# Kernel tuning notes

Hardware: AMD Instinct MI355X
Metric: run time of the kernel (lower is better)

The kernel has to match this reference:

```python
import jax, jax.numpy as jnp
import numpy as np

N = 100000      # nodes
E = 2500000     # edges
DIN, H, DOUT = 3, 32, 4
EPS = 1e-5

def _lin(k, i, o):
    kw, kb = jax.random.split(k)
    lim = 1.0 / np.sqrt(i)
    W = jax.random.uniform(kw, (i, o), jnp.float32, -lim, lim)
    b = jax.random.uniform(kb, (o,), jnp.float32, -lim, lim)
    return W, b

def setup_inputs():
    key = jax.random.key(0)
    ks = jax.random.split(key, 12)
    x = jax.random.normal(ks[0], (N, DIN), jnp.float32)
    edge_index = jax.random.randint(ks[1], (2, E), 0, N, dtype=jnp.int32)
    w_in1, b_in1 = _lin(ks[2], DIN, H)
    w_in2, b_in2 = _lin(ks[3], H, H)
    gamma = jnp.ones((H,), jnp.float32)
    beta = jnp.zeros((H,), jnp.float32)
    wg1, bg1 = _lin(ks[4], H, H)
    wg2, bg2 = _lin(ks[5], H, H)
    wg3, bg3 = _lin(ks[6], H, H)
    wo1, bo1 = _lin(ks[7], H, H)
    wo2, bo2 = _lin(ks[8], H, H)
    wo3, bo3 = _lin(ks[9], H, DOUT)
    return dict(x=x, w_in1=w_in1, b_in1=b_in1, w_in2=w_in2, b_in2=b_in2,
                gamma=gamma, beta=beta,
                wg1=wg1, bg1=bg1, wg2=wg2, bg2=bg2, wg3=wg3, bg3=bg3,
                wo1=wo1, bo1=bo1, wo2=wo2, bo2=bo2, wo3=wo3, bo3=bo3,
                edge_index=edge_index)

def _gcn(h, W, b, src, dst, norm):
    # PyG GCNConv: x' = scatter_add(norm * (xW)[src] -> dst) + bias
    hw = h @ W                                   # [N, H]
    msg = hw[src] * norm[:, None]                # [E+N, H] gather + scale
    out = jax.ops.segment_sum(msg, dst, num_segments=N)
    return out + b

def reference(x, w_in1, b_in1, w_in2, b_in2, gamma, beta,
              wg1, bg1, wg2, bg2, wg3, bg3,
              wo1, bo1, wo2, bo2, wo3, bo3, edge_index):
    leaky = lambda v: jax.nn.leaky_relu(v, 0.01)
    # input MLP
    h = leaky(x @ w_in1 + b_in1)
    h = leaky(h @ w_in2 + b_in2)
    # BatchNorm1d (training-mode batch statistics, biased variance)
    mu = jnp.mean(h, axis=0)
    var = jnp.mean((h - mu) ** 2, axis=0)
    h = (h - mu) * jax.lax.rsqrt(var + EPS) * gamma + beta
    # gcn_norm with self-loops: deg over target index, sym normalization
    loop = jnp.arange(N, dtype=edge_index.dtype)
    src = jnp.concatenate([edge_index[0], loop])
    dst = jnp.concatenate([edge_index[1], loop])
    deg = jax.ops.segment_sum(jnp.ones_like(src, jnp.float32), dst, num_segments=N)
    dis = jax.lax.rsqrt(deg)                     # deg >= 1 due to self-loops
    norm = dis[src] * dis[dst]                   # [E+N]
    h = jax.nn.elu(_gcn(h, wg1, bg1, src, dst, norm))
    h = jax.nn.elu(_gcn(h, wg2, bg2, src, dst, norm))
    h = jax.nn.elu(_gcn(h, wg3, bg3, src, dst, norm))
    # output MLP
    r = leaky(h @ wo1 + bo1)
    r = leaky(r @ wo2 + bo2)
    r = r @ wo3 + bo3                            # [N, 4]
    r = r.at[:, 0].set(jax.nn.sigmoid(r[:, 0]))
    return r
```

## Files before the change

kernel.cpp:

```cpp
#include <hip/hip_runtime.h>
#include <hip/hip_fp16.h>

#define HF 32
#define EPS 1e-5f
#define BSH 7
#define BSZ 128
#define CH  16384
#define SUBCAP 512
#define CAP (8*SUBCAP)

typedef int vi4 __attribute__((ext_vector_type(4)));

__device__ __forceinline__ float leaky(float v){ return fmaxf(v, 0.01f*v); }
__device__ __forceinline__ float elu1(float v){ return v > 0.f ? v : (expf(v)-1.f); }
__device__ __forceinline__ float sigmoidf(float v){ return 1.f/(1.f+expf(-v)); }

__device__ __forceinline__ int4 nt_load_i4(const int* p){
    vi4 v = __builtin_nontemporal_load((const vi4*)p);
    return make_int4(v.x, v.y, v.z, v.w);
}

__device__ __forceinline__ void addrow8(float* a, float4 v){
    const __half2* p = (const __half2*)&v;
#pragma unroll
    for (int k = 0; k < 4; k++){
        float2 f = __half22float2(p[k]);
        a[2*k] += f.x; a[2*k+1] += f.y;
    }
}
__device__ __forceinline__ float4 h2add4f(float4 a, float4 b){
    __half2* pa = (__half2*)&a; __half2* pb = (__half2*)&b;
    float4 r; __half2* pr = (__half2*)&r;
#pragma unroll
    for (int k = 0; k < 4; k++) pr[k] = __hadd2(pa[k], pb[k]);
    return r;
}

union SMem {
    struct {
        float sW1[3*HF]; float sB1[HF]; float sW2[HF*HF]; float sB2[HF];
        float sh[256][33];
    } mlp;
    struct { int lcnt[1024]; int lbase[1024]; int lpos[1024]; } bin;
};

__global__ __launch_bounds__(256)
void k_mlp_bin(const float* __restrict__ x,
               const float* __restrict__ w1, const float* __restrict__ b1,
               const float* __restrict__ w2, const float* __restrict__ b2,
               __half* __restrict__ h, float* __restrict__ stats,
               const int* __restrict__ src, const int* __restrict__ dst,
               int* __restrict__ gfill, int* __restrict__ ep,
               int N, int E, int B, int NB1){
    __shared__ SMem sm;
    int t = threadIdx.x;
    if ((int)blockIdx.x < NB1){
        for (int i = t; i < 3*HF; i += 256) sm.mlp.sW1[i] = w1[i];
        if (t < HF){ sm.mlp.sB1[t] = b1[t]; sm.mlp.sB2[t] = b2[t]; }
        for (int i = t; i < HF*HF; i += 256) sm.mlp.sW2[i] = w2[i];
        __syncthreads();
        int n = blockIdx.x*256 + t;
        float h2[HF];
        if (n < N){
            float x0 = x[(size_t)n*3], x1 = x[(size_t)n*3+1], x2 = x[(size_t)n*3+2];
            float h1[HF];
#pragma unroll
            for (int j = 0; j < HF; j++){
                float v = fmaf(x0, sm.mlp.sW1[j], fmaf(x1, sm.mlp.sW1[HF+j],
                          fmaf(x2, sm.mlp.sW1[2*HF+j], sm.mlp.sB1[j])));
                h1[j] = leaky(v);
            }
#pragma unroll
            for (int j = 0; j < HF; j++){
                float v = sm.mlp.sB2[j];
#pragma unroll
                for (int i = 0; i < HF; i++) v = fmaf(h1[i], sm.mlp.sW2[i*HF+j], v);
                h2[j] = leaky(v);
            }
            float4* hv = (float4*)(h + (size_t)n*HF);
#pragma unroll
            for (int jb = 0; jb < 4; jb++){
                __half2 hh[4];
#pragma unroll
                for (int k = 0; k < 4; k++)
                    hh[k] = __float22half2_rn(make_float2(h2[jb*8+2*k], h2[jb*8+2*k+1]));
                hv[jb] = *(float4*)hh;
            }
        } else {
#pragma unroll
            for (int j = 0; j < HF; j++) h2[j] = 0.f;
        }
#pragma unroll
        for (int j = 0; j < HF; j++) sm.mlp.sh[t][j] = h2[j];
        __syncthreads();
        int f = t & 31, g = t >> 5;
        float s = 0.f, ss = 0.f;
        for (int i = 0; i < 32; i++){
            float v = sm.mlp.sh[g*32 + i][f];
            s += v; ss += v*v;
        }
        __syncthreads();
        sm.mlp.sh[g][f] = s; sm.mlp.sh[8+g][f] = ss;
        __syncthreads();
        if (t < HF){
            float a = 0.f, b = 0.f;
#pragma unroll
            for (int g2 = 0; g2 < 8; g2++){ a += sm.mlp.sh[g2][t]; b += sm.mlp.sh[8+g2][t]; }
            atomicAdd(&stats[t], a);
            atomicAdd(&stats[HF+t], b);
        }
    } else {
        int bid = blockIdx.x - NB1;
        for (int i = t; i < B; i += 256){ sm.bin.lcnt[i] = 0; sm.bin.lpos[i] = 0; }
        __syncthreads();
        int base = bid * CH;
        int xcd = blockIdx.x & 7;
        bool full = (base + CH <= E);
        if (full){
            for (int i = 0; i < 16; i++){
                int4 d4 = nt_load_i4(dst + base + (t + i*256)*4);
                atomicAdd(&sm.bin.lcnt[d4.x >> BSH], 1);
                atomicAdd(&sm.bin.lcnt[d4.y >> BSH], 1);
                atomicAdd(&sm.bin.lcnt[d4.z >> BSH], 1);
                atomicAdd(&sm.bin.lcnt[d4.w >> BSH], 1);
            }
        } else {
            for (int i = 0; i < 64; i++){
                int e = base + t + i*256;
                if (e < E) atomicAdd(&sm.bin.lcnt[dst[e] >> BSH], 1);
            }
        }
        __syncthreads();
        for (int i = t; i < B; i += 256){
            int c = sm.bin.lcnt[i];
            sm.bin.lbase[i] = c ? (i*CAP + xcd*SUBCAP + atomicAdd(&gfill[i*8 + xcd], c)) : 0;
        }
        __syncthreads();
        if (full){
            for (int i = 0; i < 16; i++){
                int idx = base + (t + i*256)*4;
                int4 d4 = *(const int4*)(dst + idx);
                int4 s4 = *(const int4*)(src + idx);
                int dd[4] = {d4.x, d4.y, d4.z, d4.w};
                int ss[4] = {s4.x, s4.y, s4.z, s4.w};
#pragma unroll
                for (int k = 0; k < 4; k++){
                    int bb = dd[k] >> BSH;
                    int p = sm.bin.lbase[bb] + atomicAdd(&sm.bin.lpos[bb], 1);
                    ep[p] = (ss[k] << BSH) | (dd[k] & (BSZ-1));
                }
            }
        } else {
            for (int i = 0; i < 64; i++){
                int e = base + t + i*256;
                if (e < E){
                    int d = dst[e], s = src[e];
                    int bb = d >> BSH;
                    int p = sm.bin.lbase[bb] + atomicAdd(&sm.bin.lpos[bb], 1);
                    ep[p] = (s << BSH) | (d & (BSZ-1));
                }
            }
        }
    }
}

__global__ __launch_bounds__(256)
void k_csr_t1(int* __restrict__ ep, const int* __restrict__ gfill,
              int2* __restrict__ rowp2, float* __restrict__ dis,
              const __half* __restrict__ h, const float* __restrict__ stats,
              const float* __restrict__ gamma, const float* __restrict__ beta,
              const float* __restrict__ W, __half* __restrict__ tout,
              int N, int B){
    __shared__ int sep[CAP];
    __shared__ int lcnt[128], lpre[128], lfill[128];
    __shared__ float sW[HF*HF];
    __shared__ float sscale[HF], sshift[HF];
    int t = threadIdx.x;
    int b = blockIdx.x;
    for (int i = t; i < HF*HF; i += 256) sW[i] = W[i];
    if (t < HF){
        float inv = 1.0f/(float)N;
        float mu  = stats[t]*inv;
        float var = stats[HF+t]*inv - mu*mu;
        float rs  = rsqrtf(var + EPS);
        float sc  = rs*gamma[t];
        sscale[t] = sc;
        sshift[t] = beta[t] - mu*sc;
    }
    if (t < 128){ lcnt[t] = 0; lfill[t] = 0; }
    int cx[8], coff[8], cnt = 0;
#pragma unroll
    for (int xx = 0; xx < 8; xx++){ cx[xx] = gfill[b*8 + xx]; coff[xx] = cnt; cnt += cx[xx]; }
    int base = b*CAP;
    __syncthreads();
#pragma unroll
    for (int xx = 0; xx < 8; xx++)
        for (int j = t; j < cx[xx]; j += 256) sep[coff[xx] + j] = ep[base + xx*SUBCAP + j];
    __syncthreads();
    for (int e = t; e < cnt; e += 256) atomicAdd(&lcnt[sep[e] & (BSZ-1)], 1);
    __syncthreads();
    if (t < 128){
        int dg = lcnt[t];
        int pre = 0;
        for (int j = 0; j < t; j++) pre += lcnt[j];
        lpre[t] = pre;
        int n = b*BSZ + t;
        if (n < N){
            rowp2[n] = make_int2(base + pre, base + pre + dg);
            dis[n]   = rsqrtf((float)dg + 1.0f);
        }
    }
    __syncthreads();
    for (int e = t; e < cnt; e += 256){
        int val = sep[e];
        int d = val & (BSZ-1);
        int p = lpre[d] + atomicAdd(&lfill[d], 1);
        ep[base + p] = val >> BSH;
    }
    int nloc = t >> 1, fh = (t & 1) * 16;
    int n = b*BSZ + nloc;
    if (n < N){
        float dloc = rsqrtf((float)lcnt[nloc] + 1.0f);
        const float4* hv4 = (const float4*)h + (size_t)n*4;
        float v[HF];
#pragma unroll
        for (int k = 0; k < 4; k++){
            float4 raw = hv4[k];
            const __half2* p2 = (const __half2*)&raw;
#pragma unroll
            for (int q = 0; q < 4; q++){
                float2 f2 = __half22float2(p2[q]);
                v[8*k + 2*q]     = f2.x;
                v[8*k + 2*q + 1] = f2.y;
            }
        }
#pragma unroll
        for (int f = 0; f < HF; f++) v[f] = fmaf(v[f], sscale[f], sshift[f]);
        float o[16];
#pragma unroll
        for (int j = 0; j < 16; j++) o[j] = 0.f;
#pragma unroll
        for (int i = 0; i < HF; i++){
            float vi = v[i];
#pragma unroll
            for (int j4 = 0; j4 < 4; j4++){
                float4 w4 = *(const float4*)&sW[i*HF + fh + 4*j4];
                o[4*j4]   = fmaf(vi, w4.x, o[4*j4]);
                o[4*j4+1] = fmaf(vi, w4.y, o[4*j4+1]);
                o[4*j4+2] = fmaf(vi, w4.z, o[4*j4+2]);
                o[4*j4+3] = fmaf(vi, w4.w, o[4*j4+3]);
            }
        }
        float4* ov = (float4*)tout + (size_t)n*4 + (t & 1)*2;
#pragma unroll
        for (int k = 0; k < 2; k++){
            __half2 hh[4];
#pragma unroll
            for (int q = 0; q < 4; q++)
                hh[q] = __float22half2_rn(make_float2(o[8*k+2*q]*dloc, o[8*k+2*q+1]*dloc));
            ov[k] = *(float4*)hh;
        }
    }
}

__global__ __launch_bounds__(256)
void k_gather_t(const __half* __restrict__ tin, const int* __restrict__ esrc,
                const int2* __restrict__ rowp2, const float* __restrict__ dis,
                const float* __restrict__ bias, const float* __restrict__ W,
                __half* __restrict__ tout, int N){
    __shared__ float sW[HF*HF];
    __shared__ float sh[32][33];
    int tid = threadIdx.x;
    for (int i = tid; i < HF*HF; i += 256) sW[i] = W[i];
    int node = tid >> 3, l2 = tid & 7, l = l2 & 3, hf = l2 >> 2;
    int n = blockIdx.x*32 + node;
    float acc[8] = {0.f,0.f,0.f,0.f,0.f,0.f,0.f,0.f};
    float d = 0.f;
    const float4* tv = (const float4*)tin;
    if (n < N){
        if (hf == 0) addrow8(acc, tv[(size_t)n*4 + l]);
        int2 r = rowp2[n];
        int e0 = r.x, e1 = r.y;
        int ea = (e0 + 3) & ~3; if (ea > e1) ea = e1;
        if (hf == 0) for (int e = e0; e < ea; e++) addrow8(acc, tv[(size_t)esrc[e]*4 + l]);
        int nch = (e1 - ea) >> 2;
        int c = hf;
        if (c + 2 < nch){
            int4 a4 = nt_load_i4(&esrc[ea + 4*c]);
            int4 b4 = nt_load_i4(&esrc[ea + 4*(c+2)]);
            while (true){
                int cn = c + 4;
                bool more = (cn + 2 < nch);
                int4 na4, nb4;
                if (more){
                    na4 = nt_load_i4(&esrc[ea + 4*cn]);
                    nb4 = nt_load_i4(&esrc[ea + 4*(cn+2)]);
                }
                float4 v0 = tv[(size_t)a4.x*4 + l];
                float4 v1 = tv[(size_t)a4.y*4 + l];
                float4 v2 = tv[(size_t)a4.z*4 + l];
                float4 v3 = tv[(size_t)a4.w*4 + l];
                float4 v4 = tv[(size_t)b4.x*4 + l];
                float4 v5 = tv[(size_t)b4.y*4 + l];
                float4 v6 = tv[(size_t)b4.z*4 + l];
                float4 v7 = tv[(size_t)b4.w*4 + l];
                addrow8(acc, h2add4f(h2add4f(v0, v1), h2add4f(v2, v3)));
                addrow8(acc, h2add4f(h2add4f(v4, v5), h2add4f(v6, v7)));
                c = cn;
                if (!more) break;
                a4 = na4; b4 = nb4;
            }
        }
        for (; c < nch; c += 2){
            int4 s4 = nt_load_i4(&esrc[ea + 4*c]);
            float4 v0 = tv[(size_t)s4.x*4 + l];
            float4 v1 = tv[(size_t)s4.y*4 + l];
            float4 v2 = tv[(size_t)s4.z*4 + l];
            float4 v3 = tv[(size_t)s4.w*4 + l];
            addrow8(acc, h2add4f(h2add4f(v0, v1), h2add4f(v2, v3)));
        }
        if (hf == 1) for (int e = ea + 4*nch; e < e1; e++) addrow8(acc, tv[(size_t)esrc[e]*4 + l]);
#pragma unroll
        for (int cc = 0; cc < 8; cc++) acc[cc] += __shfl_xor(acc[cc], 4);
        d = dis[n];
#pragma unroll
        for (int cc = 0; cc < 8; cc++)
            acc[cc] = elu1(fmaf(d, acc[cc], bias[8*l + cc]));
    }
    __syncthreads();
    if (hf == 0){
#pragma unroll
        for (int cc = 0; cc < 8; cc++) sh[node][8*l + cc] = acc[cc];
    }
    __syncthreads();
    float o[4] = {0.f,0.f,0.f,0.f};
#pragma unroll
    for (int i = 0; i < HF; i++){
        float hvv = sh[node][i];
        float4 w4 = *(const float4*)&sW[i*HF + 4*l2];
        o[0] = fmaf(hvv, w4.x, o[0]); o[1] = fmaf(hvv, w4.y, o[1]);
        o[2] = fmaf(hvv, w4.z, o[2]); o[3] = fmaf(hvv, w4.w, o[3]);
    }
    if (n < N){
        __half2 hh[2];
        hh[0] = __float22half2_rn(make_float2(o[0]*d, o[1]*d));
        hh[1] = __float22half2_rn(make_float2(o[2]*d, o[3]*d));
        ((float2*)tout)[(size_t)n*8 + l2] = *(float2*)hh;
    }
}

__global__ __launch_bounds__(256)
void k_gather_out(const __half* __restrict__ tin, const int* __restrict__ esrc,
                  const int2* __restrict__ rowp2, const float* __restrict__ dis,
                  const float* __restrict__ bg3,
                  const float* __restrict__ wo1, const float* __restrict__ bo1,
                  const float* __restrict__ wo2, const float* __restrict__ bo2,
                  const float* __restrict__ wo3, const float* __restrict__ bo3,
                  float* __restrict__ out, int N){
    __shared__ float sW1[HF*HF], sW2[HF*HF], sW3[HF*4];
    __shared__ float sh[32][33], sh2[32][33];
    int tid = threadIdx.x;
    for (int i = tid; i < HF*HF; i += 256){ sW1[i] = wo1[i]; sW2[i] = wo2[i]; }
    if (tid < HF*4) sW3[tid] = wo3[tid];
    int node = tid >> 3, l2 = tid & 7, l = l2 & 3, hf = l2 >> 2;
    int n = blockIdx.x*32 + node;
    float acc[8] = {0.f,0.f,0.f,0.f,0.f,0.f,0.f,0.f};
    const float4* tv = (const float4*)tin;
    if (n < N){
        if (hf == 0) addrow8(acc, tv[(size_t)n*4 + l]);
        int2 r = rowp2[n];
        int e0 = r.x, e1 = r.y;
        int ea = (e0 + 3) & ~3; if (ea > e1) ea = e1;
        if (hf == 0) for (int e = e0; e < ea; e++) addrow8(acc, tv[(size_t)esrc[e]*4 + l]);
        int nch = (e1 - ea) >> 2;
        int c = hf;
        if (c + 2 < nch){
            int4 a4 = nt_load_i4(&esrc[ea + 4*c]);
            int4 b4 = nt_load_i4(&esrc[ea + 4*(c+2)]);
            while (true){
                int cn = c + 4;
                bool more = (cn + 2 < nch);
                int4 na4, nb4;
                if (more){
                    na4 = nt_load_i4(&esrc[ea + 4*cn]);
                    nb4 = nt_load_i4(&esrc[ea + 4*(cn+2)]);
                }
                float4 v0 = tv[(size_t)a4.x*4 + l];
                float4 v1 = tv[(size_t)a4.y*4 + l];
                float4 v2 = tv[(size_t)a4.z*4 + l];
                float4 v3 = tv[(size_t)a4.w*4 + l];
                float4 v4 = tv[(size_t)b4.x*4 + l];
                float4 v5 = tv[(size_t)b4.y*4 + l];
                float4 v6 = tv[(size_t)b4.z*4 + l];
                float4 v7 = tv[(size_t)b4.w*4 + l];
                addrow8(acc, h2add4f(h2add4f(v0, v1), h2add4f(v2, v3)));
                addrow8(acc, h2add4f(h2add4f(v4, v5), h2add4f(v6, v7)));
                c = cn;
                if (!more) break;
                a4 = na4; b4 = nb4;
            }
        }
        for (; c < nch; c += 2){
            int4 s4 = nt_load_i4(&esrc[ea + 4*c]);
            float4 v0 = tv[(size_t)s4.x*4 + l];
            float4 v1 = tv[(size_t)s4.y*4 + l];
            float4 v2 = tv[(size_t)s4.z*4 + l];
            float4 v3 = tv[(size_t)s4.w*4 + l];
            addrow8(acc, h2add4f(h2add4f(v0, v1), h2add4f(v2, v3)));
        }
        if (hf == 1) for (int e = ea + 4*nch; e < e1; e++) addrow8(acc, tv[(size_t)esrc[e]*4 + l]);
#pragma unroll
        for (int cc = 0; cc < 8; cc++) acc[cc] += __shfl_xor(acc[cc], 4);
        float d = dis[n];
#pragma unroll
        for (int cc = 0; cc < 8; cc++)
            acc[cc] = elu1(fmaf(d, acc[cc], bg3[8*l + cc]));
    }
    __syncthreads();
    if (hf == 0){
#pragma unroll
        for (int cc = 0; cc < 8; cc++) sh[node][8*l + cc] = acc[cc];
    }
    __syncthreads();
    float o1[4];
#pragma unroll
    for (int cc = 0; cc < 4; cc++) o1[cc] = bo1[4*l2 + cc];
#pragma unroll
    for (int i = 0; i < HF; i++){
        float hvv = sh[node][i];
        float4 w4 = *(const float4*)&sW1[i*HF + 4*l2];
        o1[0] = fmaf(hvv, w4.x, o1[0]); o1[1] = fmaf(hvv, w4.y, o1[1]);
        o1[2] = fmaf(hvv, w4.z, o1[2]); o1[3] = fmaf(hvv, w4.w, o1[3]);
    }
#pragma unroll
    for (int cc = 0; cc < 4; cc++) sh2[node][4*l2 + cc] = leaky(o1[cc]);
    __syncthreads();
    float o2[4];
#pragma unroll
    for (int cc = 0; cc < 4; cc++) o2[cc] = bo2[4*l2 + cc];
#pragma unroll
    for (int i = 0; i < HF; i++){
        float hvv = sh2[node][i];
        float4 w4 = *(const float4*)&sW2[i*HF + 4*l2];
        o2[0] = fmaf(hvv, w4.x, o2[0]); o2[1] = fmaf(hvv, w4.y, o2[1]);
        o2[2] = fmaf(hvv, w4.z, o2[2]); o2[3] = fmaf(hvv, w4.w, o2[3]);
    }
    __syncthreads();
#pragma unroll
    for (int cc = 0; cc < 4; cc++) sh[node][4*l2 + cc] = leaky(o2[cc]);
    __syncthreads();
    if (n < N && l2 < 4){
        float v = bo3[l2];
#pragma unroll
        for (int i = 0; i < HF; i++) v = fmaf(sh[node][i], sW3[i*4 + l2], v);
        if (l2 == 0) v = sigmoidf(v);
        out[(size_t)n*4 + l2] = v;
    }
}

extern "C" void kernel_launch(void* const* d_in, const int* in_sizes, int n_in,
                              void* d_out, int out_size, void* d_ws, size_t ws_size,
                              hipStream_t stream) {
    const float* x     = (const float*)d_in[0];
    const float* w_in1 = (const float*)d_in[1];
    const float* b_in1 = (const float*)d_in[2];
    const float* w_in2 = (const float*)d_in[3];
    const float* b_in2 = (const float*)d_in[4];
    const float* gamma = (const float*)d_in[5];
    const float* beta  = (const float*)d_in[6];
    const float* wg1   = (const float*)d_in[7];
    const float* bg1   = (const float*)d_in[8];
    const float* wg2   = (const float*)d_in[9];
    const float* bg2   = (const float*)d_in[10];
    const float* wg3   = (const float*)d_in[11];
    const float* bg3   = (const float*)d_in[12];
    const float* wo1   = (const float*)d_in[13];
    const float* bo1   = (const float*)d_in[14];
    const float* wo2   = (const float*)d_in[15];
    const float* bo2   = (const float*)d_in[16];
    const float* wo3   = (const float*)d_in[17];
    const float* bo3   = (const float*)d_in[18];
    const int*   ei    = (const int*)d_in[19];

    int N = in_sizes[0] / 3;
    int E = in_sizes[19] / 2;
    int B = (N + BSZ - 1) >> BSH;

    char* w = (char*)d_ws;
    size_t o = 0;
    auto alloc = [&](size_t bytes){ size_t r = o; o = (o + bytes + 255) & ~(size_t)255; return r; };
    float* stats = (float*)(w + alloc(2*HF*sizeof(float)));
    int*   gfill = (int*)  (w + alloc((size_t)B*8*4));
    size_t zero_bytes = o;
    int2*  rowp2 = (int2*) (w + alloc((size_t)N*8));
    float* dis   = (float*)(w + alloc((size_t)N*4));
    int*   ep    = (int*)  (w + alloc((size_t)B*CAP*4));
    __half* bufH = (__half*)(w + alloc((size_t)N*HF*2));
    __half* tA   = (__half*)(w + alloc((size_t)N*HF*2));
    __half* tB   = (__half*)(w + alloc((size_t)N*HF*2));

    hipMemsetAsync(d_ws, 0, zero_bytes, stream);

    const int* src = ei;
    const int* dst = ei + E;
    int NB1 = (N + 255) / 256;
    int NC  = (E + CH - 1) / CH;
    int GN  = (N + 31) / 32;

    k_mlp_bin<<<NB1 + NC, 256, 0, stream>>>(x, w_in1, b_in1, w_in2, b_in2, bufH, stats,
                                            src, dst, gfill, ep, N, E, B, NB1);
    k_csr_t1<<<B, 256, 0, stream>>>(ep, gfill, rowp2, dis,
                                    bufH, stats, gamma, beta, wg1, tA, N, B);
    k_gather_t<<<GN, 256, 0, stream>>>(tA, ep, rowp2, dis, bg1, wg2, tB, N);
    k_gather_t<<<GN, 256, 0, stream>>>(tB, ep, rowp2, dis, bg2, wg3, tA, N);
    k_gather_out<<<GN, 256, 0, stream>>>(tA, ep, rowp2, dis, bg3,
                                         wo1, bo1, wo2, bo2, wo3, bo3, (float*)d_out, N);
}
```

Measured before the change: 291.9 us.

## Fuse all stages into one persistent kernel with software grid barriers

```diff
diff --git a/kernel.cpp b/kernel.cpp
--- a/kernel.cpp
+++ b/kernel.cpp
@@ -36,266 +36,359 @@
     return r;
 }
 
-union SMem {
+union FSM {
     struct {
         float sW1[3*HF]; float sB1[HF]; float sW2[HF*HF]; float sB2[HF];
         float sh[256][33];
     } mlp;
     struct { int lcnt[1024]; int lbase[1024]; int lpos[1024]; } bin;
+    struct {
+        int sep[CAP]; int lcnt[128]; int lpre[128]; int lfill[128];
+        float sW[HF*HF]; float sscale[HF]; float sshift[HF];
+    } csr;
+    struct { float sW[HF*HF]; float sh[32][33]; } gt;
+    struct { float sW1[HF*HF]; float sW2[HF*HF]; float sW3[HF*4];
+             float sh[32][33]; float sh2[32][33]; } go;
 };
 
-__global__ __launch_bounds__(256)
-void k_mlp_bin(const float* __restrict__ x,
-               const float* __restrict__ w1, const float* __restrict__ b1,
-               const float* __restrict__ w2, const float* __restrict__ b2,
-               __half* __restrict__ h, float* __restrict__ stats,
-               const int* __restrict__ src, const int* __restrict__ dst,
-               int* __restrict__ gfill, int* __restrict__ ep,
-               int N, int E, int B, int NB1){
-    __shared__ SMem sm;
+__device__ __forceinline__ void grid_bar(int* cnt, int* gen){
+    __syncthreads();
+    if (threadIdx.x == 0){
+        __threadfence();
+        int g = __hip_atomic_load(gen, __ATOMIC_RELAXED, __HIP_MEMORY_SCOPE_AGENT);
+        int prev = __hip_atomic_fetch_add(cnt, 1, __ATOMIC_ACQ_REL, __HIP_MEMORY_SCOPE_AGENT);
+        if (prev == (int)gridDim.x - 1){
+            __hip_atomic_store(cnt, 0, __ATOMIC_RELAXED, __HIP_MEMORY_SCOPE_AGENT);
+            __hip_atomic_fetch_add(gen, 1, __ATOMIC_RELEASE, __HIP_MEMORY_SCOPE_AGENT);
+        } else {
+            while (__hip_atomic_load(gen, __ATOMIC_ACQUIRE, __HIP_MEMORY_SCOPE_AGENT) == g)
+                __builtin_amdgcn_s_sleep(2);
+        }
+        __threadfence();
+    }
+    __syncthreads();
+}
+
+__global__ __launch_bounds__(256, 4)
+void k_fused(const float* __restrict__ x,
+             const float* __restrict__ w_in1, const float* __restrict__ b_in1,
+             const float* __restrict__ w_in2, const float* __restrict__ b_in2,
+             const float* __restrict__ gamma, const float* __restrict__ beta,
+             const float* __restrict__ wg1, const float* __restrict__ bg1,
+             const float* __restrict__ wg2, const float* __restrict__ bg2,
+             const float* __restrict__ wg3, const float* __restrict__ bg3,
+             const float* __restrict__ wo1, const float* __restrict__ bo1,
+             const float* __restrict__ wo2, const float* __restrict__ bo2,
+             const float* __restrict__ wo3, const float* __restrict__ bo3,
+             const int* __restrict__ src, const int* __restrict__ dst,
+             float* __restrict__ stats, int* __restrict__ gfill,
+             int* __restrict__ barv,
+             int2* __restrict__ rowp2, float* __restrict__ dis, int* __restrict__ ep,
+             __half* __restrict__ bufH, __half* __restrict__ tA, __half* __restrict__ tB,
+             float* __restrict__ out,
+             int N, int E, int B, int NC, int NB1, int GN)
+{
+    __shared__ FSM sm;
     int t = threadIdx.x;
-    if ((int)blockIdx.x < NB1){
-        for (int i = t; i < 3*HF; i += 256) sm.mlp.sW1[i] = w1[i];
-        if (t < HF){ sm.mlp.sB1[t] = b1[t]; sm.mlp.sB2[t] = b2[t]; }
-        for (int i = t; i < HF*HF; i += 256) sm.mlp.sW2[i] = w2[i];
-        __syncthreads();
-        int n = blockIdx.x*256 + t;
-        float h2[HF];
-        if (n < N){
-            float x0 = x[(size_t)n*3], x1 = x[(size_t)n*3+1], x2 = x[(size_t)n*3+2];
-            float h1[HF];
-#pragma unroll
-            for (int j = 0; j < HF; j++){
-                float v = fmaf(x0, sm.mlp.sW1[j], fmaf(x1, sm.mlp.sW1[HF+j],
-                          fmaf(x2, sm.mlp.sW1[2*HF+j], sm.mlp.sB1[j])));
-                h1[j] = leaky(v);
-            }
-#pragma unroll
-            for (int j = 0; j < HF; j++){
-                float v = sm.mlp.sB2[j];
-#pragma unroll
-                for (int i = 0; i < HF; i++) v = fmaf(h1[i], sm.mlp.sW2[i*HF+j], v);
-                h2[j] = leaky(v);
-            }
-            float4* hv = (float4*)(h + (size_t)n*HF);
-#pragma unroll
-            for (int jb = 0; jb < 4; jb++){
-                __half2 hh[4];
-#pragma unroll
-                for (int k = 0; k < 4; k++)
-                    hh[k] = __float22half2_rn(make_float2(h2[jb*8+2*k], h2[jb*8+2*k+1]));
-                hv[jb] = *(float4*)hh;
+    int blk = blockIdx.x, nblk = gridDim.x;
+
+    for (int w = blk; w < NC + NB1; w += nblk){
+        __syncthreads();
+        if (w < NC){
+            int bid = w;
+            for (int i = t; i < B; i += 256){ sm.bin.lcnt[i] = 0; sm.bin.lpos[i] = 0; }
+            __syncthreads();
+            int base = bid * CH;
+            int xcd = bid & 7;
+            bool full = (base + CH <= E);
+            if (full){
+                for (int i = 0; i < 16; i++){
+                    int4 d4 = nt_load_i4(dst + base + (t + i*256)*4);
+                    atomicAdd(&sm.bin.lcnt[d4.x >> BSH], 1);
+                    atomicAdd(&sm.bin.lcnt[d4.y >> BSH], 1);
+                    atomicAdd(&sm.bin.lcnt[d4.z >> BSH], 1);
+                    atomicAdd(&sm.bin.lcnt[d4.w >> BSH], 1);
+                }
+            } else {
+                for (int i = 0; i < 64; i++){
+                    int e = base + t + i*256;
+                    if (e < E) atomicAdd(&sm.bin.lcnt[dst[e] >> BSH], 1);
+                }
+            }
+            __syncthreads();
+            for (int i = t; i < B; i += 256){
+                int c = sm.bin.lcnt[i];
+                sm.bin.lbase[i] = c ? (i*CAP + xcd*SUBCAP + atomicAdd(&gfill[i*8 + xcd], c)) : 0;
+            }
+            __syncthreads();
+            if (full){
+                for (int i = 0; i < 16; i++){
+                    int idx = base + (t + i*256)*4;
+                    int4 d4 = *(const int4*)(dst + idx);
+                    int4 s4 = *(const int4*)(src + idx);
+                    int dd[4] = {d4.x, d4.y, d4.z, d4.w};
+                    int ss[4] = {s4.x, s4.y, s4.z, s4.w};
+#pragma unroll
+                    for (int k = 0; k < 4; k++){
+                        int bb = dd[k] >> BSH;
+                        int p = sm.bin.lbase[bb] + atomicAdd(&sm.bin.lpos[bb], 1);
+                        ep[p] = (ss[k] << BSH) | (dd[k] & (BSZ-1));
+                    }
+                }
+            } else {
+                for (int i = 0; i < 64; i++){
+                    int e = base + t + i*256;
+                    if (e < E){
+                        int d = dst[e], s = src[e];
+                        int bb = d >> BSH;
+                        int p = sm.bin.lbase[bb] + atomicAdd(&sm.bin.lpos[bb], 1);
+                        ep[p] = (s << BSH) | (d & (BSZ-1));
+                    }
+                }
             }
         } else {
-#pragma unroll
-            for (int j = 0; j < HF; j++) h2[j] = 0.f;
-        }
-#pragma unroll
-        for (int j = 0; j < HF; j++) sm.mlp.sh[t][j] = h2[j];
-        __syncthreads();
-        int f = t & 31, g = t >> 5;
-        float s = 0.f, ss = 0.f;
-        for (int i = 0; i < 32; i++){
-            float v = sm.mlp.sh[g*32 + i][f];
-            s += v; ss += v*v;
-        }
-        __syncthreads();
-        sm.mlp.sh[g][f] = s; sm.mlp.sh[8+g][f] = ss;
-        __syncthreads();
-        if (t < HF){
-            float a = 0.f, b = 0.f;
-#pragma unroll
-            for (int g2 = 0; g2 < 8; g2++){ a += sm.mlp.sh[g2][t]; b += sm.mlp.sh[8+g2][t]; }
-            atomicAdd(&stats[t], a);
-            atomicAdd(&stats[HF+t], b);
-        }
-    } else {
-        int bid = blockIdx.x - NB1;
-        for (int i = t; i < B; i += 256){ sm.bin.lcnt[i] = 0; sm.bin.lpos[i] = 0; }
-        __syncthreads();
-        int base = bid * CH;
-        int xcd = blockIdx.x & 7;
-        bool full = (base + CH <= E);
-        if (full){
-            for (int i = 0; i < 16; i++){
-                int4 d4 = nt_load_i4(dst + base + (t + i*256)*4);
-                atomicAdd(&sm.bin.lcnt[d4.x >> BSH], 1);
-                atomicAdd(&sm.bin.lcnt[d4.y >> BSH], 1);
-                atomicAdd(&sm.bin.lcnt[d4.z >> BSH], 1);
-                atomicAdd(&sm.bin.lcnt[d4.w >> BSH], 1);
-            }
-        } else {
-            for (int i = 0; i < 64; i++){
-                int e = base + t + i*256;
-                if (e < E) atomicAdd(&sm.bin.lcnt[dst[e] >> BSH], 1);
-            }
-        }
-        __syncthreads();
-        for (int i = t; i < B; i += 256){
-            int c = sm.bin.lcnt[i];
-            sm.bin.lbase[i] = c ? (i*CAP + xcd*SUBCAP + atomicAdd(&gfill[i*8 + xcd], c)) : 0;
-        }
-        __syncthreads();
-        if (full){
-            for (int i = 0; i < 16; i++){
-                int idx = base + (t + i*256)*4;
-                int4 d4 = *(const int4*)(dst + idx);
-                int4 s4 = *(const int4*)(src + idx);
-                int dd[4] = {d4.x, d4.y, d4.z, d4.w};
-                int ss[4] = {s4.x, s4.y, s4.z, s4.w};
-#pragma unroll
-                for (int k = 0; k < 4; k++){
-                    int bb = dd[k] >> BSH;
-                    int p = sm.bin.lbase[bb] + atomicAdd(&sm.bin.lpos[bb], 1);
-                    ep[p] = (ss[k] << BSH) | (dd[k] & (BSZ-1));
-                }
-            }
-        } else {
-            for (int i = 0; i < 64; i++){
-                int e = base + t + i*256;
-                if (e < E){
-                    int d = dst[e], s = src[e];
-                    int bb = d >> BSH;
-                    int p = sm.bin.lbase[bb] + atomicAdd(&sm.bin.lpos[bb], 1);
-                    ep[p] = (s << BSH) | (d & (BSZ-1));
-                }
-            }
-        }
-    }
-}
-
-__global__ __launch_bounds__(256)
-void k_csr_t1(int* __restrict__ ep, const int* __restrict__ gfill,
-              int2* __restrict__ rowp2, float* __restrict__ dis,
-              const __half* __restrict__ h, const float* __restrict__ stats,
-              const float* __restrict__ gamma, const float* __restrict__ beta,
-              const float* __restrict__ W, __half* __restrict__ tout,
-              int N, int B){
-    __shared__ int sep[CAP];
-    __shared__ int lcnt[128], lpre[128], lfill[128];
-    __shared__ float sW[HF*HF];
-    __shared__ float sscale[HF], sshift[HF];
-    int t = threadIdx.x;
-    int b = blockIdx.x;
-    for (int i = t; i < HF*HF; i += 256) sW[i] = W[i];
+            for (int i = t; i < 3*HF; i += 256) sm.mlp.sW1[i] = w_in1[i];
+            if (t < HF){ sm.mlp.sB1[t] = b_in1[t]; sm.mlp.sB2[t] = b_in2[t]; }
+            for (int i = t; i < HF*HF; i += 256) sm.mlp.sW2[i] = w_in2[i];
+            __syncthreads();
+            int n = (w - NC)*256 + t;
+            float h2[HF];
+            if (n < N){
+                float x0 = x[(size_t)n*3], x1 = x[(size_t)n*3+1], x2 = x[(size_t)n*3+2];
+                float h1[HF];
+#pragma unroll
+                for (int j = 0; j < HF; j++){
+                    float v = fmaf(x0, sm.mlp.sW1[j], fmaf(x1, sm.mlp.sW1[HF+j],
+                              fmaf(x2, sm.mlp.sW1[2*HF+j], sm.mlp.sB1[j])));
+                    h1[j] = leaky(v);
+                }
+#pragma unroll
+                for (int j = 0; j < HF; j++){
+                    float v = sm.mlp.sB2[j];
+#pragma unroll
+                    for (int i = 0; i < HF; i++) v = fmaf(h1[i], sm.mlp.sW2[i*HF+j], v);
+                    h2[j] = leaky(v);
+                }
+                float4* hv = (float4*)(bufH + (size_t)n*HF);
+#pragma unroll
+                for (int jb = 0; jb < 4; jb++){
+                    __half2 hh[4];
+#pragma unroll
+                    for (int k = 0; k < 4; k++)
+                        hh[k] = __float22half2_rn(make_float2(h2[jb*8+2*k], h2[jb*8+2*k+1]));
+                    hv[jb] = *(float4*)hh;
+                }
+            } else {
+#pragma unroll
+                for (int j = 0; j < HF; j++) h2[j] = 0.f;
+            }
+#pragma unroll
+            for (int j = 0; j < HF; j++) sm.mlp.sh[t][j] = h2[j];
+            __syncthreads();
+            int f = t & 31, g = t >> 5;
+            float s = 0.f, ss = 0.f;
+            for (int i = 0; i < 32; i++){
+                float v = sm.mlp.sh[g*32 + i][f];
+                s += v; ss += v*v;
+            }
+            __syncthreads();
+            sm.mlp.sh[g][f] = s; sm.mlp.sh[8+g][f] = ss;
+            __syncthreads();
+            if (t < HF){
+                float a = 0.f, b = 0.f;
+#pragma unroll
+                for (int g2 = 0; g2 < 8; g2++){ a += sm.mlp.sh[g2][t]; b += sm.mlp.sh[8+g2][t]; }
+                atomicAdd(&stats[t], a);
+                atomicAdd(&stats[HF+t], b);
+            }
+        }
+    }
+    grid_bar(barv, barv + 64);
+
+    for (int i = t; i < HF*HF; i += 256) sm.csr.sW[i] = wg1[i];
     if (t < HF){
         float inv = 1.0f/(float)N;
         float mu  = stats[t]*inv;
         float var = stats[HF+t]*inv - mu*mu;
         float rs  = rsqrtf(var + EPS);
         float sc  = rs*gamma[t];
-        sscale[t] = sc;
-        sshift[t] = beta[t] - mu*sc;
-    }
-    if (t < 128){ lcnt[t] = 0; lfill[t] = 0; }
-    int cx[8], coff[8], cnt = 0;
-#pragma unroll
-    for (int xx = 0; xx < 8; xx++){ cx[xx] = gfill[b*8 + xx]; coff[xx] = cnt; cnt += cx[xx]; }
-    int base = b*CAP;
-    __syncthreads();
-#pragma unroll
-    for (int xx = 0; xx < 8; xx++)
-        for (int j = t; j < cx[xx]; j += 256) sep[coff[xx] + j] = ep[base + xx*SUBCAP + j];
-    __syncthreads();
-    for (int e = t; e < cnt; e += 256) atomicAdd(&lcnt[sep[e] & (BSZ-1)], 1);
-    __syncthreads();
-    if (t < 128){
-        int dg = lcnt[t];
-        int pre = 0;
-        for (int j = 0; j < t; j++) pre += lcnt[j];
-        lpre[t] = pre;
-        int n = b*BSZ + t;
+        sm.csr.sscale[t] = sc;
+        sm.csr.sshift[t] = beta[t] - mu*sc;
+    }
+    for (int b = blk; b < B; b += nblk){
+        __syncthreads();
+        if (t < 128){ sm.csr.lcnt[t] = 0; sm.csr.lfill[t] = 0; }
+        int cx[8], coff[8], cnt = 0;
+#pragma unroll
+        for (int xx = 0; xx < 8; xx++){ cx[xx] = gfill[b*8 + xx]; coff[xx] = cnt; cnt += cx[xx]; }
+        int base = b*CAP;
+        __syncthreads();
+#pragma unroll
+        for (int xx = 0; xx < 8; xx++)
+            for (int j = t; j < cx[xx]; j += 256) sm.csr.sep[coff[xx] + j] = ep[base + xx*SUBCAP + j];
+        __syncthreads();
+        for (int e = t; e < cnt; e += 256) atomicAdd(&sm.csr.lcnt[sm.csr.sep[e] & (BSZ-1)], 1);
+        __syncthreads();
+        if (t < 128){
+            int dg = sm.csr.lcnt[t];
+            int pre = 0;
+            for (int j = 0; j < t; j++) pre += sm.csr.lcnt[j];
+            sm.csr.lpre[t] = pre;
+            int n = b*BSZ + t;
+            if (n < N){
+                rowp2[n] = make_int2(base + pre, base + pre + dg);
+                dis[n]   = rsqrtf((float)dg + 1.0f);
+            }
+        }
+        __syncthreads();
+        for (int e = t; e < cnt; e += 256){
+            int val = sm.csr.sep[e];
+            int d2 = val & (BSZ-1);
+            int p = sm.csr.lpre[d2] + atomicAdd(&sm.csr.lfill[d2], 1);
+            ep[base + p] = val >> BSH;
+        }
+        int nloc = t >> 1, fh = (t & 1) * 16;
+        int n = b*BSZ + nloc;
         if (n < N){
-            rowp2[n] = make_int2(base + pre, base + pre + dg);
-            dis[n]   = rsqrtf((float)dg + 1.0f);
-        }
-    }
-    __syncthreads();
-    for (int e = t; e < cnt; e += 256){
-        int val = sep[e];
-        int d = val & (BSZ-1);
-        int p = lpre[d] + atomicAdd(&lfill[d], 1);
-        ep[base + p] = val >> BSH;
-    }
-    int nloc = t >> 1, fh = (t & 1) * 16;
-    int n = b*BSZ + nloc;
-    if (n < N){
-        float dloc = rsqrtf((float)lcnt[nloc] + 1.0f);
-        const float4* hv4 = (const float4*)h + (size_t)n*4;
-        float v[HF];
-#pragma unroll
-        for (int k = 0; k < 4; k++){
-            float4 raw = hv4[k];
-            const __half2* p2 = (const __half2*)&raw;
-#pragma unroll
-            for (int q = 0; q < 4; q++){
-                float2 f2 = __half22float2(p2[q]);
-                v[8*k + 2*q]     = f2.x;
-                v[8*k + 2*q + 1] = f2.y;
-            }
-        }
-#pragma unroll
-        for (int f = 0; f < HF; f++) v[f] = fmaf(v[f], sscale[f], sshift[f]);
-        float o[16];
-#pragma unroll
-        for (int j = 0; j < 16; j++) o[j] = 0.f;
-#pragma unroll
-        for (int i = 0; i < HF; i++){
-            float vi = v[i];
-#pragma unroll
-            for (int j4 = 0; j4 < 4; j4++){
-                float4 w4 = *(const float4*)&sW[i*HF + fh + 4*j4];
-                o[4*j4]   = fmaf(vi, w4.x, o[4*j4]);
-                o[4*j4+1] = fmaf(vi, w4.y, o[4*j4+1]);
-                o[4*j4+2] = fmaf(vi, w4.z, o[4*j4+2]);
-                o[4*j4+3] = fmaf(vi, w4.w, o[4*j4+3]);
-            }
-        }
-        float4* ov = (float4*)tout + (size_t)n*4 + (t & 1)*2;
-#pragma unroll
-        for (int k = 0; k < 2; k++){
-            __half2 hh[4];
-#pragma unroll
-            for (int q = 0; q < 4; q++)
-                hh[q] = __float22half2_rn(make_float2(o[8*k+2*q]*dloc, o[8*k+2*q+1]*dloc));
-            ov[k] = *(float4*)hh;
-        }
-    }
-}
-
-__global__ __launch_bounds__(256)
-void k_gather_t(const __half* __restrict__ tin, const int* __restrict__ esrc,
-                const int2* __restrict__ rowp2, const float* __restrict__ dis,
-                const float* __restrict__ bias, const float* __restrict__ W,
-                __half* __restrict__ tout, int N){
-    __shared__ float sW[HF*HF];
-    __shared__ float sh[32][33];
-    int tid = threadIdx.x;
-    for (int i = tid; i < HF*HF; i += 256) sW[i] = W[i];
-    int node = tid >> 3, l2 = tid & 7, l = l2 & 3, hf = l2 >> 2;
-    int n = blockIdx.x*32 + node;
-    float acc[8] = {0.f,0.f,0.f,0.f,0.f,0.f,0.f,0.f};
-    float d = 0.f;
-    const float4* tv = (const float4*)tin;
-    if (n < N){
-        if (hf == 0) addrow8(acc, tv[(size_t)n*4 + l]);
-        int2 r = rowp2[n];
-        int e0 = r.x, e1 = r.y;
-        int ea = (e0 + 3) & ~3; if (ea > e1) ea = e1;
-        if (hf == 0) for (int e = e0; e < ea; e++) addrow8(acc, tv[(size_t)esrc[e]*4 + l]);
-        int nch = (e1 - ea) >> 2;
-        int c = hf;
-        if (c + 2 < nch){
-            int4 a4 = nt_load_i4(&esrc[ea + 4*c]);
-            int4 b4 = nt_load_i4(&esrc[ea + 4*(c+2)]);
-            while (true){
-                int cn = c + 4;
-                bool more = (cn + 2 < nch);
-                int4 na4, nb4;
-                if (more){
-                    na4 = nt_load_i4(&esrc[ea + 4*cn]);
-                    nb4 = nt_load_i4(&esrc[ea + 4*(cn+2)]);
-                }
+            float dloc = rsqrtf((float)sm.csr.lcnt[nloc] + 1.0f);
+            const float4* hv4 = (const float4*)bufH + (size_t)n*4;
+            float v[HF];
+#pragma unroll
+            for (int k = 0; k < 4; k++){
+                float4 raw = hv4[k];
+                const __half2* p2 = (const __half2*)&raw;
+#pragma unroll
+                for (int q = 0; q < 4; q++){
+                    float2 f2 = __half22float2(p2[q]);
+                    v[8*k + 2*q]     = f2.x;
+                    v[8*k + 2*q + 1] = f2.y;
+                }
+            }
+#pragma unroll
+            for (int f = 0; f < HF; f++) v[f] = fmaf(v[f], sm.csr.sscale[f], sm.csr.sshift[f]);
+            float o[16];
+#pragma unroll
+            for (int j = 0; j < 16; j++) o[j] = 0.f;
+#pragma unroll
+            for (int i = 0; i < HF; i++){
+                float vi = v[i];
+#pragma unroll
+                for (int j4 = 0; j4 < 4; j4++){
+                    float4 w4 = *(const float4*)&sm.csr.sW[i*HF + fh + 4*j4];
+                    o[4*j4]   = fmaf(vi, w4.x, o[4*j4]);
+                    o[4*j4+1] = fmaf(vi, w4.y, o[4*j4+1]);
+                    o[4*j4+2] = fmaf(vi, w4.z, o[4*j4+2]);
+                    o[4*j4+3] = fmaf(vi, w4.w, o[4*j4+3]);
+                }
+            }
+            float4* ov = (float4*)tA + (size_t)n*4 + (t & 1)*2;
+#pragma unroll
+            for (int k = 0; k < 2; k++){
+                __half2 hh[4];
+#pragma unroll
+                for (int q = 0; q < 4; q++)
+                    hh[q] = __float22half2_rn(make_float2(o[8*k+2*q]*dloc, o[8*k+2*q+1]*dloc));
+                ov[k] = *(float4*)hh;
+            }
+        }
+    }
+    grid_bar(barv, barv + 64);
+
+    {
+        const __half* gin = tA; __half* gouth = tB;
+        const float* gbias = bg1; const float* gw = wg2;
+        for (int layer = 0; layer < 2; layer++){
+            for (int i = t; i < HF*HF; i += 256) sm.gt.sW[i] = gw[i];
+            for (int c = blk; c < GN; c += nblk){
+                __syncthreads();
+                int node = t >> 3, l2 = t & 7, l = l2 & 3, hfv = l2 >> 2;
+                int n = c*32 + node;
+                float acc[8] = {0.f,0.f,0.f,0.f,0.f,0.f,0.f,0.f};
+                float d = 0.f;
+                const float4* tv = (const float4*)gin;
+                if (n < N){
+                    if (hfv == 0) addrow8(acc, tv[(size_t)n*4 + l]);
+                    int2 r = rowp2[n];
+                    int e0 = r.x, e1 = r.y;
+                    int ea = (e0 + 3) & ~3; if (ea > e1) ea = e1;
+                    if (hfv == 0) for (int e = e0; e < ea; e++) addrow8(acc, tv[(size_t)ep[e]*4 + l]);
+                    int nch = (e1 - ea) >> 2;
+                    int c2 = hfv;
+                    for (; c2 + 2 < nch; c2 += 4){
+                        int4 a4 = nt_load_i4(&ep[ea + 4*c2]);
+                        int4 b4 = nt_load_i4(&ep[ea + 4*(c2+2)]);
+                        float4 v0 = tv[(size_t)a4.x*4 + l];
+                        float4 v1 = tv[(size_t)a4.y*4 + l];
+                        float4 v2 = tv[(size_t)a4.z*4 + l];
+                        float4 v3 = tv[(size_t)a4.w*4 + l];
+                        float4 v4 = tv[(size_t)b4.x*4 + l];
+                        float4 v5 = tv[(size_t)b4.y*4 + l];
+                        float4 v6 = tv[(size_t)b4.z*4 + l];
+                        float4 v7 = tv[(size_t)b4.w*4 + l];
+                        addrow8(acc, h2add4f(h2add4f(v0, v1), h2add4f(v2, v3)));
+                        addrow8(acc, h2add4f(h2add4f(v4, v5), h2add4f(v6, v7)));
+                    }
+                    for (; c2 < nch; c2 += 2){
+                        int4 s4 = nt_load_i4(&ep[ea + 4*c2]);
+                        float4 v0 = tv[(size_t)s4.x*4 + l];
+                        float4 v1 = tv[(size_t)s4.y*4 + l];
+                        float4 v2 = tv[(size_t)s4.z*4 + l];
+                        float4 v3 = tv[(size_t)s4.w*4 + l];
+                        addrow8(acc, h2add4f(h2add4f(v0, v1), h2add4f(v2, v3)));
+                    }
+                    if (hfv == 1) for (int e = ea + 4*nch; e < e1; e++) addrow8(acc, tv[(size_t)ep[e]*4 + l]);
+#pragma unroll
+                    for (int cc = 0; cc < 8; cc++) acc[cc] += __shfl_xor(acc[cc], 4);
+                    d = dis[n];
+#pragma unroll
+                    for (int cc = 0; cc < 8; cc++)
+                        acc[cc] = elu1(fmaf(d, acc[cc], gbias[8*l + cc]));
+                }
+                __syncthreads();
+                if (hfv == 0){
+#pragma unroll
+                    for (int cc = 0; cc < 8; cc++) sm.gt.sh[node][8*l + cc] = acc[cc];
+                }
+                __syncthreads();
+                float o[4] = {0.f,0.f,0.f,0.f};
+#pragma unroll
+                for (int i = 0; i < HF; i++){
+                    float hvv = sm.gt.sh[node][i];
+                    float4 w4 = *(const float4*)&sm.gt.sW[i*HF + 4*l2];
+                    o[0] = fmaf(hvv, w4.x, o[0]); o[1] = fmaf(hvv, w4.y, o[1]);
+                    o[2] = fmaf(hvv, w4.z, o[2]); o[3] = fmaf(hvv, w4.w, o[3]);
+                }
+                if (n < N){
+                    __half2 hh[2];
+                    hh[0] = __float22half2_rn(make_float2(o[0]*d, o[1]*d));
+                    hh[1] = __float22half2_rn(make_float2(o[2]*d, o[3]*d));
+                    ((float2*)gouth)[(size_t)n*8 + l2] = *(float2*)hh;
+                }
+            }
+            grid_bar(barv, barv + 64);
+            gin = tB; gouth = tA; gbias = bg2; gw = wg3;
+        }
+    }
+
+    for (int i = t; i < HF*HF; i += 256){ sm.go.sW1[i] = wo1[i]; sm.go.sW2[i] = wo2[i]; }
+    if (t < HF*4) sm.go.sW3[t] = wo3[t];
+    for (int c = blk; c < GN; c += nblk){
+        __syncthreads();
+        int node = t >> 3, l2 = t & 7, l = l2 & 3, hfv = l2 >> 2;
+        int n = c*32 + node;
+        float acc[8] = {0.f,0.f,0.f,0.f,0.f,0.f,0.f,0.f};
+        const float4* tv = (const float4*)tA;
+        if (n < N){
+            if (hfv == 0) addrow8(acc, tv[(size_t)n*4 + l]);
+            int2 r = rowp2[n];
+            int e0 = r.x, e1 = r.y;
+            int ea = (e0 + 3) & ~3; if (ea > e1) ea = e1;
+            if (hfv == 0) for (int e = e0; e < ea; e++) addrow8(acc, tv[(size_t)ep[e]*4 + l]);
+            int nch = (e1 - ea) >> 2;
+            int c2 = hfv;
+            for (; c2 + 2 < nch; c2 += 4){
+                int4 a4 = nt_load_i4(&ep[ea + 4*c2]);
+                int4 b4 = nt_load_i4(&ep[ea + 4*(c2+2)]);
                 float4 v0 = tv[(size_t)a4.x*4 + l];
                 float4 v1 = tv[(size_t)a4.y*4 + l];
                 float4 v2 = tv[(size_t)a4.z*4 + l];
@@ -306,155 +399,63 @@
                 float4 v7 = tv[(size_t)b4.w*4 + l];
                 addrow8(acc, h2add4f(h2add4f(v0, v1), h2add4f(v2, v3)));
                 addrow8(acc, h2add4f(h2add4f(v4, v5), h2add4f(v6, v7)));
-                c = cn;
-                if (!more) break;
-                a4 = na4; b4 = nb4;
-            }
-        }
-        for (; c < nch; c += 2){
-            int4 s4 = nt_load_i4(&esrc[ea + 4*c]);
-            float4 v0 = tv[(size_t)s4.x*4 + l];
-            float4 v1 = tv[(size_t)s4.y*4 + l];
-            float4 v2 = tv[(size_t)s4.z*4 + l];
-            float4 v3 = tv[(size_t)s4.w*4 + l];
-            addrow8(acc, h2add4f(h2add4f(v0, v1), h2add4f(v2, v3)));
-        }
-        if (hf == 1) for (int e = ea + 4*nch; e < e1; e++) addrow8(acc, tv[(size_t)esrc[e]*4 + l]);
-#pragma unroll
-        for (int cc = 0; cc < 8; cc++) acc[cc] += __shfl_xor(acc[cc], 4);
-        d = dis[n];
-#pragma unroll
-        for (int cc = 0; cc < 8; cc++)
-            acc[cc] = elu1(fmaf(d, acc[cc], bias[8*l + cc]));
-    }
-    __syncthreads();
-    if (hf == 0){
-#pragma unroll
-        for (int cc = 0; cc < 8; cc++) sh[node][8*l + cc] = acc[cc];
-    }
-    __syncthreads();
-    float o[4] = {0.f,0.f,0.f,0.f};
-#pragma unroll
-    for (int i = 0; i < HF; i++){
-        float hvv = sh[node][i];
-        float4 w4 = *(const float4*)&sW[i*HF + 4*l2];
-        o[0] = fmaf(hvv, w4.x, o[0]); o[1] = fmaf(hvv, w4.y, o[1]);
-        o[2] = fmaf(hvv, w4.z, o[2]); o[3] = fmaf(hvv, w4.w, o[3]);
-    }
-    if (n < N){
-        __half2 hh[2];
-        hh[0] = __float22half2_rn(make_float2(o[0]*d, o[1]*d));
-        hh[1] = __float22half2_rn(make_float2(o[2]*d, o[3]*d));
-        ((float2*)tout)[(size_t)n*8 + l2] = *(float2*)hh;
-    }
-}
-
-__global__ __launch_bounds__(256)
-void k_gather_out(const __half* __restrict__ tin, const int* __restrict__ esrc,
-                  const int2* __restrict__ rowp2, const float* __restrict__ dis,
-                  const float* __restrict__ bg3,
-                  const float* __restrict__ wo1, const float* __restrict__ bo1,
-                  const float* __restrict__ wo2, const float* __restrict__ bo2,
-                  const float* __restrict__ wo3, const float* __restrict__ bo3,
-                  float* __restrict__ out, int N){
-    __shared__ float sW1[HF*HF], sW2[HF*HF], sW3[HF*4];
-    __shared__ float sh[32][33], sh2[32][33];
-    int tid = threadIdx.x;
-    for (int i = tid; i < HF*HF; i += 256){ sW1[i] = wo1[i]; sW2[i] = wo2[i]; }
-    if (tid < HF*4) sW3[tid] = wo3[tid];
-    int node = tid >> 3, l2 = tid & 7, l = l2 & 3, hf = l2 >> 2;
-    int n = blockIdx.x*32 + node;
-    float acc[8] = {0.f,0.f,0.f,0.f,0.f,0.f,0.f,0.f};
-    const float4* tv = (const float4*)tin;
-    if (n < N){
-        if (hf == 0) addrow8(acc, tv[(size_t)n*4 + l]);
-        int2 r = rowp2[n];
-        int e0 = r.x, e1 = r.y;
-        int ea = (e0 + 3) & ~3; if (ea > e1) ea = e1;
-        if (hf == 0) for (int e = e0; e < ea; e++) addrow8(acc, tv[(size_t)esrc[e]*4 + l]);
-        int nch = (e1 - ea) >> 2;
-        int c = hf;
-        if (c + 2 < nch){
-            int4 a4 = nt_load_i4(&esrc[ea + 4*c]);
-            int4 b4 = nt_load_i4(&esrc[ea + 4*(c+2)]);
-            while (true){
-                int cn = c + 4;
-                bool more = (cn + 2 < nch);
-                int4 na4, nb4;
-                if (more){
-                    na4 = nt_load_i4(&esrc[ea + 4*cn]);
-                    nb4 = nt_load_i4(&esrc[ea + 4*(cn+2)]);
-                }
-                float4 v0 = tv[(size_t)a4.x*4 + l];
-                float4 v1 = tv[(size_t)a4.y*4 + l];
-                float4 v2 = tv[(size_t)a4.z*4 + l];
-                float4 v3 = tv[(size_t)a4.w*4 + l];
-                float4 v4 = tv[(size_t)b4.x*4 + l];
-                float4 v5 = tv[(size_t)b4.y*4 + l];
-                float4 v6 = tv[(size_t)b4.z*4 + l];
-                float4 v7 = tv[(size_t)b4.w*4 + l];
+            }
+            for (; c2 < nch; c2 += 2){
+                int4 s4 = nt_load_i4(&ep[ea + 4*c2]);
+                float4 v0 = tv[(size_t)s4.x*4 + l];
+                float4 v1 = tv[(size_t)s4.y*4 + l];
+                float4 v2 = tv[(size_t)s4.z*4 + l];
+                float4 v3 = tv[(size_t)s4.w*4 + l];
                 addrow8(acc, h2add4f(h2add4f(v0, v1), h2add4f(v2, v3)));
-                addrow8(acc, h2add4f(h2add4f(v4, v5), h2add4f(v6, v7)));
-                c = cn;
-                if (!more) break;
-                a4 = na4; b4 = nb4;
-            }
-        }
-        for (; c < nch; c += 2){
-            int4 s4 = nt_load_i4(&esrc[ea + 4*c]);
-            float4 v0 = tv[(size_t)s4.x*4 + l];
-            float4 v1 = tv[(size_t)s4.y*4 + l];
-            float4 v2 = tv[(size_t)s4.z*4 + l];
-            float4 v3 = tv[(size_t)s4.w*4 + l];
-            addrow8(acc, h2add4f(h2add4f(v0, v1), h2add4f(v2, v3)));
-        }
-        if (hf == 1) for (int e = ea + 4*nch; e < e1; e++) addrow8(acc, tv[(size_t)esrc[e]*4 + l]);
-#pragma unroll
-        for (int cc = 0; cc < 8; cc++) acc[cc] += __shfl_xor(acc[cc], 4);
-        float d = dis[n];
-#pragma unroll
-        for (int cc = 0; cc < 8; cc++)
-            acc[cc] = elu1(fmaf(d, acc[cc], bg3[8*l + cc]));
-    }
-    __syncthreads();
-    if (hf == 0){
-#pragma unroll
-        for (int cc = 0; cc < 8; cc++) sh[node][8*l + cc] = acc[cc];
-    }
-    __syncthreads();
-    float o1[4];
-#pragma unroll
-    for (int cc = 0; cc < 4; cc++) o1[cc] = bo1[4*l2 + cc];
-#pragma unroll
-    for (int i = 0; i < HF; i++){
-        float hvv = sh[node][i];
-        float4 w4 = *(const float4*)&sW1[i*HF + 4*l2];
-        o1[0] = fmaf(hvv, w4.x, o1[0]); o1[1] = fmaf(hvv, w4.y, o1[1]);
-        o1[2] = fmaf(hvv, w4.z, o1[2]); o1[3] = fmaf(hvv, w4.w, o1[3]);
-    }
-#pragma unroll
-    for (int cc = 0; cc < 4; cc++) sh2[node][4*l2 + cc] = leaky(o1[cc]);
-    __syncthreads();
-    float o2[4];
-#pragma unroll
-    for (int cc = 0; cc < 4; cc++) o2[cc] = bo2[4*l2 + cc];
-#pragma unroll
-    for (int i = 0; i < HF; i++){
-        float hvv = sh2[node][i];
-        float4 w4 = *(const float4*)&sW2[i*HF + 4*l2];
-        o2[0] = fmaf(hvv, w4.x, o2[0]); o2[1] = fmaf(hvv, w4.y, o2[1]);
-        o2[2] = fmaf(hvv, w4.z, o2[2]); o2[3] = fmaf(hvv, w4.w, o2[3]);
-    }
-    __syncthreads();
-#pragma unroll
-    for (int cc = 0; cc < 4; cc++) sh[node][4*l2 + cc] = leaky(o2[cc]);
-    __syncthreads();
-    if (n < N && l2 < 4){
-        float v = bo3[l2];
-#pragma unroll
-        for (int i = 0; i < HF; i++) v = fmaf(sh[node][i], sW3[i*4 + l2], v);
-        if (l2 == 0) v = sigmoidf(v);
-        out[(size_t)n*4 + l2] = v;
+            }
+            if (hfv == 1) for (int e = ea + 4*nch; e < e1; e++) addrow8(acc, tv[(size_t)ep[e]*4 + l]);
+#pragma unroll
+            for (int cc = 0; cc < 8; cc++) acc[cc] += __shfl_xor(acc[cc], 4);
+            float d = dis[n];
+#pragma unroll
+            for (int cc = 0; cc < 8; cc++)
+                acc[cc] = elu1(fmaf(d, acc[cc], bg3[8*l + cc]));
+        }
+        __syncthreads();
+        if (hfv == 0){
+#pragma unroll
+            for (int cc = 0; cc < 8; cc++) sm.go.sh[node][8*l + cc] = acc[cc];
+        }
+        __syncthreads();
+        float o1[4];
+#pragma unroll
+        for (int cc = 0; cc < 4; cc++) o1[cc] = bo1[4*l2 + cc];
+#pragma unroll
+        for (int i = 0; i < HF; i++){
+            float hvv = sm.go.sh[node][i];
+            float4 w4 = *(const float4*)&sm.go.sW1[i*HF + 4*l2];
+            o1[0] = fmaf(hvv, w4.x, o1[0]); o1[1] = fmaf(hvv, w4.y, o1[1]);
+            o1[2] = fmaf(hvv, w4.z, o1[2]); o1[3] = fmaf(hvv, w4.w, o1[3]);
+        }
+#pragma unroll
+        for (int cc = 0; cc < 4; cc++) sm.go.sh2[node][4*l2 + cc] = leaky(o1[cc]);
+        __syncthreads();
+        float o2[4];
+#pragma unroll
+        for (int cc = 0; cc < 4; cc++) o2[cc] = bo2[4*l2 + cc];
+#pragma unroll
+        for (int i = 0; i < HF; i++){
+            float hvv = sm.go.sh2[node][i];
+            float4 w4 = *(const float4*)&sm.go.sW2[i*HF + 4*l2];
+            o2[0] = fmaf(hvv, w4.x, o2[0]); o2[1] = fmaf(hvv, w4.y, o2[1]);
+            o2[2] = fmaf(hvv, w4.z, o2[2]); o2[3] = fmaf(hvv, w4.w, o2[3]);
+        }
+        __syncthreads();
+#pragma unroll
+        for (int cc = 0; cc < 4; cc++) sm.go.sh[node][4*l2 + cc] = leaky(o2[cc]);
+        __syncthreads();
+        if (n < N && l2 < 4){
+            float v = bo3[l2];
+#pragma unroll
+            for (int i = 0; i < HF; i++) v = fmaf(sm.go.sh[node][i], sm.go.sW3[i*4 + l2], v);
+            if (l2 == 0) v = sigmoidf(v);
+            out[(size_t)n*4 + l2] = v;
+        }
     }
 }
 
@@ -491,6 +492,7 @@
     auto alloc = [&](size_t bytes){ size_t r = o; o = (o + bytes + 255) & ~(size_t)255; return r; };
     float* stats = (float*)(w + alloc(2*HF*sizeof(float)));
     int*   gfill = (int*)  (w + alloc((size_t)B*8*4));
+    int*   barv  = (int*)  (w + alloc(512));
     size_t zero_bytes = o;
     int2*  rowp2 = (int2*) (w + alloc((size_t)N*8));
     float* dis   = (float*)(w + alloc((size_t)N*4));
@@ -507,12 +509,24 @@
     int NC  = (E + CH - 1) / CH;
     int GN  = (N + 31) / 32;
 
-    k_mlp_bin<<<NB1 + NC, 256, 0, stream>>>(x, w_in1, b_in1, w_in2, b_in2, bufH, stats,
-                                            src, dst, gfill, ep, N, E, B, NB1);
-    k_csr_t1<<<B, 256, 0, stream>>>(ep, gfill, rowp2, dis,
-                                    bufH, stats, gamma, beta, wg1, tA, N, B);
-    k_gather_t<<<GN, 256, 0, stream>>>(tA, ep, rowp2, dis, bg1, wg2, tB, N);
-    k_gather_t<<<GN, 256, 0, stream>>>(tB, ep, rowp2, dis, bg2, wg3, tA, N);
-    k_gather_out<<<GN, 256, 0, stream>>>(tA, ep, rowp2, dis, bg3,
-                                         wo1, bo1, wo2, bo2, wo3, bo3, (float*)d_out, N);
+    static int s_nblk = 0;
+    if (s_nblk == 0){
+        int ncu = 256;
+        hipDeviceProp_t prop;
+        if (hipGetDeviceProperties(&prop, 0) == hipSuccess && prop.multiProcessorCount > 0)
+            ncu = prop.multiProcessorCount;
+        int nb = 0;
+        if (hipOccupancyMaxActiveBlocksPerMultiprocessor(&nb, k_fused, 256, 0) != hipSuccess || nb < 1)
+            nb = 2;
+        long g = (long)ncu * nb;
+        if (g > 2048) g = 2048;
+        s_nblk = (int)g;
+    }
+
+    k_fused<<<s_nblk, 256, 0, stream>>>(x, w_in1, b_in1, w_in2, b_in2, gamma, beta,
+                                        wg1, bg1, wg2, bg2, wg3, bg3,
+                                        wo1, bo1, wo2, bo2, wo3, bo3,
+                                        src, dst, stats, gfill, barv,
+                                        rowp2, dis, ep, bufH, tA, tB,
+                                        (float*)d_out, N, E, B, NC, NB1, GN);
 }
```

Measured after the change: 964.5 us. +230.4%, slower.
